# Optimization experiments

Measured on AMD Instinct MI355X. Metric: run time of the kernel, lower is better.

Reference implementation:

```python
import jax, jax.numpy as jnp
import numpy as np

B, S, E, H = 4, 1024, 1024, 16
HD = E // H

def setup_inputs() -> dict:
    key = jax.random.key(0)
    ks = jax.random.split(key, 12)
    std = 1.0 / np.sqrt(E)
    inp = {
        "query": jax.random.normal(ks[0], (B, S, E), jnp.float32),
        "key_t": jax.random.normal(ks[1], (B, S, E), jnp.float32),
        "value": jax.random.normal(ks[2], (B, S, E), jnp.float32),
        # causal mask, broadcastable to (B, H, S, S); 0 => masked
        "mask": jnp.tril(jnp.ones((S, S), jnp.int32))[None, None],
        "Wq": jax.random.normal(ks[3], (E, E), jnp.float32) * std,
        "bq": jnp.zeros((E,), jnp.float32),
        "Wk": jax.random.normal(ks[4], (E, E), jnp.float32) * std,
        "bk": jnp.zeros((E,), jnp.float32),
        "Wv": jax.random.normal(ks[5], (E, E), jnp.float32) * std,
        "bv": jnp.zeros((E,), jnp.float32),
        "Wo": jax.random.normal(ks[6], (E, E), jnp.float32) * std,
        "bo": jnp.zeros((E,), jnp.float32),
    }
    return inp

def reference(query, key_t, value, mask, Wq, bq, Wk, bk, Wv, bv, Wo, bo):
    scale = jnp.asarray(np.sqrt(HD), query.dtype)
    # projections (torch Linear: x @ W.T + b), split into heads -> (B, H, S, HD)
    def split_heads(x):
        return x.reshape(B, S, H, HD).transpose(0, 2, 1, 3)
    q = split_heads(query @ Wq.T + bq)
    k = split_heads(key_t @ Wk.T + bk)
    v = split_heads(value @ Wv.T + bv)
    scores = jnp.einsum("bhqd,bhkd->bhqk", q, k) / scale  # (B,H,S,S)
    scores = jnp.where(mask == 0, jnp.asarray(-jnp.inf, scores.dtype), scores)
    attn = jax.nn.softmax(scores, axis=-1)
    # dropout is identity in eval / p=0
    out = jnp.einsum("bhqk,bhkd->bhqd", attn, v)
    out = out.transpose(0, 2, 1, 3).reshape(B, S, E)
    out = out @ Wo.T + bo
    return out, attn
```

## Files before the change

### kernel.cpp

```cpp
#include <hip/hip_runtime.h>
#include <hip/hip_bf16.h>


typedef short bf16x8 __attribute__((ext_vector_type(8)));
typedef float f32x4 __attribute__((ext_vector_type(4)));

__device__ __forceinline__ unsigned short f2bf(float f) {
  union { float f; unsigned u; } v; v.f = f;
  unsigned r = v.u + 0x7FFF + ((v.u >> 16) & 1);
  return (unsigned short)(r >> 16);
}

__device__ __forceinline__ void gload16(const unsigned short* g, unsigned short* l) {
  __builtin_amdgcn_global_load_lds(
      (const __attribute__((address_space(1))) unsigned int*)g,
      (__attribute__((address_space(3))) unsigned int*)l, 16, 0, 0);
}

__global__ __launch_bounds__(256) void cast3_k(
    const float* __restrict__ a, const float* __restrict__ b,
    const float* __restrict__ c,
    unsigned short* __restrict__ oa, unsigned short* __restrict__ ob,
    unsigned short* __restrict__ oc) {
  const float* in = blockIdx.y == 0 ? a : blockIdx.y == 1 ? b : c;
  unsigned short* out = blockIdx.y == 0 ? oa : blockIdx.y == 1 ? ob : oc;
  int i = (blockIdx.x * 256 + threadIdx.x) * 8;
  float4 x = *(const float4*)(in + i);
  float4 y = *(const float4*)(in + i + 4);
  unsigned short t[8] = { f2bf(x.x), f2bf(x.y), f2bf(x.z), f2bf(x.w),
                          f2bf(y.x), f2bf(y.y), f2bf(y.z), f2bf(y.w) };
  *(bf16x8*)(out + i) = *(bf16x8*)t;
}

__global__ __launch_bounds__(256) void cast4_k(
    const float* __restrict__ a, const float* __restrict__ b,
    const float* __restrict__ c, const float* __restrict__ d,
    unsigned short* __restrict__ oa, unsigned short* __restrict__ ob,
    unsigned short* __restrict__ oc, unsigned short* __restrict__ od) {
  const float* in = blockIdx.y == 0 ? a : blockIdx.y == 1 ? b : blockIdx.y == 2 ? c : d;
  unsigned short* out = blockIdx.y == 0 ? oa : blockIdx.y == 1 ? ob : blockIdx.y == 2 ? oc : od;
  int i = (blockIdx.x * 256 + threadIdx.x) * 8;
  float4 x = *(const float4*)(in + i);
  float4 y = *(const float4*)(in + i + 4);
  unsigned short t[8] = { f2bf(x.x), f2bf(x.y), f2bf(x.z), f2bf(x.w),
                          f2bf(y.x), f2bf(y.y), f2bf(y.z), f2bf(y.w) };
  *(bf16x8*)(out + i) = *(bf16x8*)t;
}

__device__ __forceinline__ void gemm_core(
    const unsigned short* __restrict__ A, const unsigned short* __restrict__ W,
    int m0, int n0, int K, unsigned short* As, unsigned short* Bs, f32x4 acc[4][4])
{
  const int tid = threadIdx.x;
  const int w = tid >> 6, lane = tid & 63, quad = lane >> 4, lc = lane & 15;
  const int wm = (w >> 1) * 64, wn = (w & 1) * 64;
  const int lrow = lane >> 3, lg = lane & 7;

  for (int kb = 0; kb < K; kb += 64) {
#pragma unroll
    for (int t = 0; t < 4; t++) {
      int row = w * 32 + t * 8 + lrow;
      int gsw = lg ^ (row & 7);
      gload16(&A[(size_t)(m0 + row) * K + kb + gsw * 8], &As[(w * 32 + t * 8) * 64]);
      gload16(&W[(size_t)(n0 + row) * K + kb + gsw * 8], &Bs[(w * 32 + t * 8) * 64]);
    }
    __syncthreads();
#pragma unroll
    for (int kk = 0; kk < 2; kk++) {
      bf16x8 af[4], bfr[4];
#pragma unroll
      for (int i = 0; i < 4; i++) {
        int ra = wm + i * 16 + lc;
        af[i] = *(const bf16x8*)&As[ra * 64 + (((kk * 4 + quad) ^ (ra & 7)) * 8)];
      }
#pragma unroll
      for (int j = 0; j < 4; j++) {
        int rb = wn + j * 16 + lc;
        bfr[j] = *(const bf16x8*)&Bs[rb * 64 + (((kk * 4 + quad) ^ (rb & 7)) * 8)];
      }
#pragma unroll
      for (int i = 0; i < 4; i++)
#pragma unroll
        for (int j = 0; j < 4; j++)
          acc[i][j] = __builtin_amdgcn_mfma_f32_16x16x32_bf16(af[i], bfr[j], acc[i][j], 0, 0, 0);
    }
    __syncthreads();
  }
}

__global__ __launch_bounds__(256) void gemm_qkv(
    const unsigned short* __restrict__ Xq, const unsigned short* __restrict__ Xk,
    const unsigned short* __restrict__ Xv,
    const unsigned short* __restrict__ Wq, const unsigned short* __restrict__ Wk,
    const unsigned short* __restrict__ Wv,
    const float* __restrict__ bq, const float* __restrict__ bk, const float* __restrict__ bv,
    unsigned short* __restrict__ Qb, unsigned short* __restrict__ Kb,
    unsigned short* __restrict__ Vt)
{
  __shared__ __align__(16) unsigned short S[128 * 136];
  unsigned short* As = S;
  unsigned short* Bs = S + 128 * 64;
  const int z = blockIdx.z;
  const unsigned short* A = z == 0 ? Xq : z == 1 ? Xk : Xv;
  const unsigned short* W = z == 0 ? Wq : z == 1 ? Wk : Wv;
  const float* bias = z == 0 ? bq : z == 1 ? bk : bv;
  unsigned short* outRM = z == 0 ? Qb : Kb;
  const int m0 = blockIdx.x * 128, n0 = blockIdx.y * 128;
  const int tid = threadIdx.x;
  const int w = tid >> 6, lane = tid & 63, quad = lane >> 4, lc = lane & 15;
  const int wm = (w >> 1) * 64, wn = (w & 1) * 64;

  f32x4 acc[4][4] = {};
  gemm_core(A, W, m0, n0, 1024, As, Bs, acc);

  if (z < 2) {
#pragma unroll
    for (int j = 0; j < 4; j++) {
      int col = n0 + wn + j * 16 + lc;
      float bvl = bias[col];
#pragma unroll
      for (int i = 0; i < 4; i++)
#pragma unroll
        for (int r = 0; r < 4; r++) {
          int row = m0 + wm + i * 16 + quad * 4 + r;
          outRM[(size_t)row * 1024 + col] = f2bf(acc[i][j][r] + bvl);
        }
    }
  } else {
    unsigned short* T = S;
#pragma unroll
    for (int j = 0; j < 4; j++) {
      int col = wn + j * 16 + lc;
      float bvl = bias[n0 + col];
#pragma unroll
      for (int i = 0; i < 4; i++)
#pragma unroll
        for (int r = 0; r < 4; r++) {
          int row = wm + i * 16 + quad * 4 + r;
          T[col * 136 + (((row >> 3) ^ (col & 7)) << 3) + (row & 7)] =
              f2bf(acc[i][j][r] + bvl);
        }
    }
    __syncthreads();
    const int b_ = m0 >> 10, sb = m0 & 1023;
#pragma unroll
    for (int it = 0; it < 8; it++) {
      int cl = w * 32 + it * 4 + (lane >> 4);
      int sg = lane & 15;
      int colg = n0 + cl;
      *(bf16x8*)&Vt[((size_t)((b_ * 16 + (colg >> 6)) * 64 + (colg & 63))) * 1024 + sb + sg * 8] =
          *(const bf16x8*)&T[cl * 136 + ((sg ^ (cl & 7)) << 3)];
    }
  }
}

__global__ __launch_bounds__(256) void gemm_out(
    const unsigned short* __restrict__ A, const unsigned short* __restrict__ W,
    const float* __restrict__ bias, float* __restrict__ outf)
{
  __shared__ __align__(16) unsigned short As[128 * 64];
  __shared__ __align__(16) unsigned short Bs[128 * 64];
  const int m0 = blockIdx.x * 128, n0 = blockIdx.y * 128;
  const int tid = threadIdx.x;
  const int w = tid >> 6, lane = tid & 63, quad = lane >> 4, lc = lane & 15;
  const int wm = (w >> 1) * 64, wn = (w & 1) * 64;

  f32x4 acc[4][4] = {};
  gemm_core(A, W, m0, n0, 1024, As, Bs, acc);

#pragma unroll
  for (int j = 0; j < 4; j++) {
    int col = n0 + wn + j * 16 + lc;
    float bvl = bias[col];
#pragma unroll
    for (int i = 0; i < 4; i++)
#pragma unroll
      for (int r = 0; r < 4; r++) {
        int row = m0 + wm + i * 16 + quad * 4 + r;
        outf[(size_t)row * 1024 + col] = acc[i][j][r] + bvl;
      }
  }
}

__global__ __launch_bounds__(256) void attn_fused(
    const unsigned short* __restrict__ Qb,
    const unsigned short* __restrict__ Kb,
    const unsigned short* __restrict__ Vt,
    float* __restrict__ attn,
    unsigned short* __restrict__ O)
{
  __shared__ __align__(16) unsigned short Ks[64 * 64];
  __shared__ __align__(16) unsigned short Vs[64 * 64];
  __shared__ __align__(16) unsigned short Pl[4][16][40];
  __shared__ __align__(16) float          Ps[4][16][36];
  const int bh = blockIdx.x, b = bh >> 4, h = bh & 15;
  const int by = (int)gridDim.y - 1 - (int)blockIdx.y;
  const int q0 = by * 64;
  const int tid = threadIdx.x;
  const int w = tid >> 6, lane = tid & 63, quad = lane >> 4, lc = lane & 15;
  const int g0 = q0 + w * 16;
  const int kt_d = g0 >> 4;
  const int nch = by + 1;
  const int sr = lane >> 3, sg = lane & 7;

  const unsigned short* qp = Qb + ((size_t)(b * 1024 + g0 + lc)) * 1024 + h * 64 + quad * 8;
  bf16x8 a0 = *(const bf16x8*)qp;
  bf16x8 a1 = *(const bf16x8*)(qp + 32);

  float m_[4] = { -1e30f, -1e30f, -1e30f, -1e30f };
  float l_[4] = { 0.f, 0.f, 0.f, 0.f };

  for (int c = 0; c < nch; c++) {
    int kv0 = c * 64;
    {
      int r0 = w * 8 + sr, r1 = 32 + r0;
      gload16(&Kb[((size_t)(b * 1024 + kv0 + r0)) * 1024 + h * 64 + (sg ^ (r0 & 7)) * 8],
              &Ks[(w * 8) * 64]);
      gload16(&Kb[((size_t)(b * 1024 + kv0 + r1)) * 1024 + h * 64 + (sg ^ (r1 & 7)) * 8],
              &Ks[(32 + w * 8) * 64]);
    }
    __syncthreads();
    int tmax = kt_d - c * 4;
    int tlim = tmax < 3 ? tmax : 3;
    for (int t = 0; t <= tlim; t++) {
      int rk = t * 16 + lc;
      const unsigned short* kr = &Ks[rk * 64];
      bf16x8 b0 = *(const bf16x8*)&kr[((quad ^ (rk & 7))) * 8];
      bf16x8 b1 = *(const bf16x8*)&kr[(((quad + 4) ^ (rk & 7))) * 8];
      f32x4 cc = {};
      cc = __builtin_amdgcn_mfma_f32_16x16x32_bf16(a0, b0, cc, 0, 0, 0);
      cc = __builtin_amdgcn_mfma_f32_16x16x32_bf16(a1, b1, cc, 0, 0, 0);
      if (t < tmax) {
#pragma unroll
        for (int r = 0; r < 4; r++) {
          float s = cc[r] * 0.125f;
          float mn = fmaxf(m_[r], s);
          l_[r] = l_[r] * __expf(m_[r] - mn) + __expf(s - mn);
          m_[r] = mn;
        }
      } else {
#pragma unroll
        for (int r = 0; r < 4; r++) {
          int qr = g0 + quad * 4 + r;
          float sv = (kv0 + t * 16 + lc) > qr ? -1e30f : cc[r] * 0.125f;
          float mn = fmaxf(m_[r], sv);
          l_[r] = l_[r] * __expf(m_[r] - mn) + __expf(sv - mn);
          m_[r] = mn;
        }
      }
    }
    __syncthreads();
  }

  float mofs[4];
#pragma unroll
  for (int r = 0; r < 4; r++) {
    float mT = m_[r];
#pragma unroll
    for (int off = 1; off < 16; off <<= 1) mT = fmaxf(mT, __shfl_xor(mT, off));
    float lt = l_[r] * __expf(m_[r] - mT);
#pragma unroll
    for (int off = 1; off < 16; off <<= 1) lt += __shfl_xor(lt, off);
    mofs[r] = mT + __logf(lt);
  }

  float* arow = attn + (size_t)bh * 1024 * 1024;
  f32x4 oacc[4] = {};
  for (int c = 0; c < nch; c++) {
    int kv0 = c * 64;
    {
      int r0 = w * 8 + sr, r1 = 32 + r0;
      gload16(&Kb[((size_t)(b * 1024 + kv0 + r0)) * 1024 + h * 64 + (sg ^ (r0 & 7)) * 8],
              &Ks[(w * 8) * 64]);
      gload16(&Kb[((size_t)(b * 1024 + kv0 + r1)) * 1024 + h * 64 + (sg ^ (r1 & 7)) * 8],
              &Ks[(32 + w * 8) * 64]);
      gload16(&Vt[((size_t)(bh * 64 + r0)) * 1024 + kv0 + (sg ^ (r0 & 7)) * 8],
              &Vs[(w * 8) * 64]);
      gload16(&Vt[((size_t)(bh * 64 + r1)) * 1024 + kv0 + (sg ^ (r1 & 7)) * 8],
              &Vs[(32 + w * 8) * 64]);
    }
    __syncthreads();
    int tmax = kt_d - c * 4;
#pragma unroll
    for (int u = 0; u < 2; u++) {
      if (u * 2 <= tmax) {
#pragma unroll
        for (int t2 = 0; t2 < 2; t2++) {
          int t = u * 2 + t2;
          if (t <= tmax) {
            int rk = t * 16 + lc;
            const unsigned short* kr = &Ks[rk * 64];
            bf16x8 b0 = *(const bf16x8*)&kr[((quad ^ (rk & 7))) * 8];
            bf16x8 b1 = *(const bf16x8*)&kr[(((quad + 4) ^ (rk & 7))) * 8];
            f32x4 cc = {};
            cc = __builtin_amdgcn_mfma_f32_16x16x32_bf16(a0, b0, cc, 0, 0, 0);
            cc = __builtin_amdgcn_mfma_f32_16x16x32_bf16(a1, b1, cc, 0, 0, 0);
#pragma unroll
            for (int r = 0; r < 4; r++) {
              int qr = g0 + quad * 4 + r;
              float p = (kv0 + t * 16 + lc) > qr ? 0.f : __expf(cc[r] * 0.125f - mofs[r]);
              Ps[w][quad * 4 + r][t2 * 16 + lc] = p;
              Pl[w][quad * 4 + r][t2 * 16 + lc] = f2bf(p);
            }
          } else {
#pragma unroll
            for (int r = 0; r < 4; r++) Pl[w][quad * 4 + r][t2 * 16 + lc] = 0;
          }
        }
        bf16x8 pa = *(const bf16x8*)&Pl[w][lc][quad * 8];
#pragma unroll
        for (int j = 0; j < 4; j++) {
          int hd = j * 16 + lc;
          bf16x8 bv = *(const bf16x8*)&Vs[hd * 64 + (((u * 4 + quad) ^ (hd & 7)) * 8)];
          oacc[j] = __builtin_amdgcn_mfma_f32_16x16x32_bf16(pa, bv, oacc[j], 0, 0, 0);
        }
        int nt = tmax - u * 2 + 1; if (nt > 2) nt = 2;
        int srow = lane >> 2, cf = (lane & 3) * 4;
        float* dst = &arow[(size_t)(g0 + srow) * 1024 + kv0 + u * 32];
        *(float4*)(dst + cf) = *(const float4*)&Ps[w][srow][cf];
        if (nt == 2)
          *(float4*)(dst + 16 + cf) = *(const float4*)&Ps[w][srow][16 + cf];
      }
    }
    __syncthreads();
  }

  {
    int rr = lane >> 3, cl = lane & 7;
    float4 z = make_float4(0.f, 0.f, 0.f, 0.f);
#pragma unroll
    for (int half = 0; half < 2; half++) {
      float* rowp = &arow[(size_t)(g0 + half * 8 + rr) * 1024];
      for (int c0 = g0 + 16 + cl * 4; c0 < 1024; c0 += 32)
        *(float4*)(rowp + c0) = z;
    }
  }

  {
    unsigned short* ob = (unsigned short*)&Ps[w][0][0];
#pragma unroll
    for (int j = 0; j < 4; j++)
#pragma unroll
      for (int r = 0; r < 4; r++)
        ob[(quad * 4 + r) * 72 + j * 16 + lc] = f2bf(oacc[j][r]);
#pragma unroll
    for (int it = 0; it < 2; it++) {
      int row = it * 8 + (lane >> 3), off = (lane & 7) * 8;
      *(bf16x8*)&O[((size_t)(b * 1024 + g0 + row)) * 1024 + h * 64 + off] =
          *(const bf16x8*)&ob[row * 72 + off];
    }
  }
}

extern "C" void kernel_launch(void* const* d_in, const int* in_sizes, int n_in,
                              void* d_out, int out_size, void* d_ws, size_t ws_size,
                              hipStream_t stream) {
  const float* query = (const float*)d_in[0];
  const float* key_t = (const float*)d_in[1];
  const float* value = (const float*)d_in[2];
  const float* Wq = (const float*)d_in[4];
  const float* bq = (const float*)d_in[5];
  const float* Wk = (const float*)d_in[6];
  const float* bk = (const float*)d_in[7];
  const float* Wv = (const float*)d_in[8];
  const float* bv = (const float*)d_in[9];
  const float* Wo = (const float*)d_in[10];
  const float* bo = (const float*)d_in[11];

  unsigned short* Xq  = (unsigned short*)d_ws;
  unsigned short* Xk  = Xq  + 4194304;
  unsigned short* Xv  = Xk  + 4194304;
  unsigned short* Wqb = Xv  + 4194304;
  unsigned short* Wkb = Wqb + 1048576;
  unsigned short* Wvb = Wkb + 1048576;
  unsigned short* Wob = Wvb + 1048576;
  unsigned short* Qb  = Wob + 1048576;
  unsigned short* Kb  = Qb  + 4194304;
  unsigned short* Vtb = Kb  + 4194304;
  unsigned short* Ob  = Vtb + 4194304;

  float* outO = (float*)d_out;
  float* attn = outO + 4194304;

  cast3_k<<<dim3(2048, 3), 256, 0, stream>>>(query, key_t, value, Xq, Xk, Xv);
  cast4_k<<<dim3(512, 4), 256, 0, stream>>>(Wq, Wk, Wv, Wo, Wqb, Wkb, Wvb, Wob);

  gemm_qkv<<<dim3(32, 8, 3), 256, 0, stream>>>(Xq, Xk, Xv, Wqb, Wkb, Wvb,
                                               bq, bk, bv, Qb, Kb, Vtb);

  attn_fused<<<dim3(64, 16), 256, 0, stream>>>(Qb, Kb, Vtb, attn, Ob);

  gemm_out<<<dim3(32, 8), 256, 0, stream>>>(Ob, Wob, bo, outO);
}
```

Baseline: 469.5 us.

## Merge cast kernels, use exp2 softmax, and drop fp32 probability staging buffer

Result: no change. 472.1 us (+0.5%).

```diff
diff --git a/kernel.cpp b/kernel.cpp
--- a/kernel.cpp
+++ b/kernel.cpp
@@ -4,6 +4,8 @@
 
 typedef short bf16x8 __attribute__((ext_vector_type(8)));
 typedef float f32x4 __attribute__((ext_vector_type(4)));
+
+#define SCALE2 0.18033688011112042f
 
 __device__ __forceinline__ unsigned short f2bf(float f) {
   union { float f; unsigned u; } v; v.f = f;
@@ -11,35 +13,36 @@
   return (unsigned short)(r >> 16);
 }
 
+__device__ __forceinline__ float bf2f(unsigned short u) {
+  union { unsigned u; float f; } v; v.u = ((unsigned)u) << 16;
+  return v.f;
+}
+
 __device__ __forceinline__ void gload16(const unsigned short* g, unsigned short* l) {
   __builtin_amdgcn_global_load_lds(
       (const __attribute__((address_space(1))) unsigned int*)g,
       (__attribute__((address_space(3))) unsigned int*)l, 16, 0, 0);
 }
 
-__global__ __launch_bounds__(256) void cast3_k(
-    const float* __restrict__ a, const float* __restrict__ b,
-    const float* __restrict__ c,
-    unsigned short* __restrict__ oa, unsigned short* __restrict__ ob,
-    unsigned short* __restrict__ oc) {
-  const float* in = blockIdx.y == 0 ? a : blockIdx.y == 1 ? b : c;
-  unsigned short* out = blockIdx.y == 0 ? oa : blockIdx.y == 1 ? ob : oc;
-  int i = (blockIdx.x * 256 + threadIdx.x) * 8;
-  float4 x = *(const float4*)(in + i);
-  float4 y = *(const float4*)(in + i + 4);
-  unsigned short t[8] = { f2bf(x.x), f2bf(x.y), f2bf(x.z), f2bf(x.w),
-                          f2bf(y.x), f2bf(y.y), f2bf(y.z), f2bf(y.w) };
-  *(bf16x8*)(out + i) = *(bf16x8*)t;
-}
-
-__global__ __launch_bounds__(256) void cast4_k(
-    const float* __restrict__ a, const float* __restrict__ b,
-    const float* __restrict__ c, const float* __restrict__ d,
-    unsigned short* __restrict__ oa, unsigned short* __restrict__ ob,
-    unsigned short* __restrict__ oc, unsigned short* __restrict__ od) {
-  const float* in = blockIdx.y == 0 ? a : blockIdx.y == 1 ? b : blockIdx.y == 2 ? c : d;
-  unsigned short* out = blockIdx.y == 0 ? oa : blockIdx.y == 1 ? ob : blockIdx.y == 2 ? oc : od;
-  int i = (blockIdx.x * 256 + threadIdx.x) * 8;
+__global__ __launch_bounds__(256) void cast_all(
+    const float* __restrict__ q, const float* __restrict__ k, const float* __restrict__ v,
+    const float* __restrict__ w0, const float* __restrict__ w1,
+    const float* __restrict__ w2, const float* __restrict__ w3,
+    unsigned short* __restrict__ oq, unsigned short* __restrict__ ok,
+    unsigned short* __restrict__ ov, unsigned short* __restrict__ o0,
+    unsigned short* __restrict__ o1, unsigned short* __restrict__ o2,
+    unsigned short* __restrict__ o3) {
+  const float* in; unsigned short* out; int i;
+  if (blockIdx.y < 3) {
+    in  = blockIdx.y == 0 ? q : blockIdx.y == 1 ? k : v;
+    out = blockIdx.y == 0 ? oq : blockIdx.y == 1 ? ok : ov;
+    i = (blockIdx.x * 256 + threadIdx.x) * 8;
+  } else {
+    int ws = blockIdx.x >> 9;
+    in  = ws == 0 ? w0 : ws == 1 ? w1 : ws == 2 ? w2 : w3;
+    out = ws == 0 ? o0 : ws == 1 ? o1 : ws == 2 ? o2 : o3;
+    i = ((blockIdx.x & 511) * 256 + threadIdx.x) * 8;
+  }
   float4 x = *(const float4*)(in + i);
   float4 y = *(const float4*)(in + i + 4);
   unsigned short t[8] = { f2bf(x.x), f2bf(x.y), f2bf(x.z), f2bf(x.w),
@@ -189,15 +192,15 @@
     float* __restrict__ attn,
     unsigned short* __restrict__ O)
 {
-  __shared__ __align__(16) unsigned short Ks[64 * 64];
-  __shared__ __align__(16) unsigned short Vs[64 * 64];
-  __shared__ __align__(16) unsigned short Pl[4][16][40];
-  __shared__ __align__(16) float          Ps[4][16][36];
+  __shared__ __align__(16) unsigned short SM[10752];
+  unsigned short* Ks = SM;
+  unsigned short* Vs = SM + 4096;
   const int bh = blockIdx.x, b = bh >> 4, h = bh & 15;
   const int by = (int)gridDim.y - 1 - (int)blockIdx.y;
   const int q0 = by * 64;
   const int tid = threadIdx.x;
   const int w = tid >> 6, lane = tid & 63, quad = lane >> 4, lc = lane & 15;
+  unsigned short* Plw = SM + 8192 + w * 640;
   const int g0 = q0 + w * 16;
   const int kt_d = g0 >> 4;
   const int nch = by + 1;
@@ -233,18 +236,18 @@
       if (t < tmax) {
 #pragma unroll
         for (int r = 0; r < 4; r++) {
-          float s = cc[r] * 0.125f;
+          float s = cc[r] * SCALE2;
           float mn = fmaxf(m_[r], s);
-          l_[r] = l_[r] * __expf(m_[r] - mn) + __expf(s - mn);
+          l_[r] = l_[r] * exp2f(m_[r] - mn) + exp2f(s - mn);
           m_[r] = mn;
         }
       } else {
 #pragma unroll
         for (int r = 0; r < 4; r++) {
           int qr = g0 + quad * 4 + r;
-          float sv = (kv0 + t * 16 + lc) > qr ? -1e30f : cc[r] * 0.125f;
+          float sv = (kv0 + t * 16 + lc) > qr ? -1e30f : cc[r] * SCALE2;
           float mn = fmaxf(m_[r], sv);
-          l_[r] = l_[r] * __expf(m_[r] - mn) + __expf(sv - mn);
+          l_[r] = l_[r] * exp2f(m_[r] - mn) + exp2f(sv - mn);
           m_[r] = mn;
         }
       }
@@ -258,10 +261,10 @@
     float mT = m_[r];
 #pragma unroll
     for (int off = 1; off < 16; off <<= 1) mT = fmaxf(mT, __shfl_xor(mT, off));
-    float lt = l_[r] * __expf(m_[r] - mT);
+    float lt = l_[r] * exp2f(m_[r] - mT);
 #pragma unroll
     for (int off = 1; off < 16; off <<= 1) lt += __shfl_xor(lt, off);
-    mofs[r] = mT + __logf(lt);
+    mofs[r] = mT + __log2f(lt);
   }
 
   float* arow = attn + (size_t)bh * 1024 * 1024;
@@ -298,28 +301,34 @@
 #pragma unroll
             for (int r = 0; r < 4; r++) {
               int qr = g0 + quad * 4 + r;
-              float p = (kv0 + t * 16 + lc) > qr ? 0.f : __expf(cc[r] * 0.125f - mofs[r]);
-              Ps[w][quad * 4 + r][t2 * 16 + lc] = p;
-              Pl[w][quad * 4 + r][t2 * 16 + lc] = f2bf(p);
+              float p = (kv0 + t * 16 + lc) > qr ? 0.f
+                        : exp2f(cc[r] * SCALE2 - mofs[r]);
+              Plw[(quad * 4 + r) * 40 + t2 * 16 + lc] = f2bf(p);
             }
           } else {
 #pragma unroll
-            for (int r = 0; r < 4; r++) Pl[w][quad * 4 + r][t2 * 16 + lc] = 0;
+            for (int r = 0; r < 4; r++) Plw[(quad * 4 + r) * 40 + t2 * 16 + lc] = 0;
           }
         }
-        bf16x8 pa = *(const bf16x8*)&Pl[w][lc][quad * 8];
+        bf16x8 pa = *(const bf16x8*)&Plw[lc * 40 + quad * 8];
 #pragma unroll
         for (int j = 0; j < 4; j++) {
           int hd = j * 16 + lc;
           bf16x8 bv = *(const bf16x8*)&Vs[hd * 64 + (((u * 4 + quad) ^ (hd & 7)) * 8)];
           oacc[j] = __builtin_amdgcn_mfma_f32_16x16x32_bf16(pa, bv, oacc[j], 0, 0, 0);
         }
-        int nt = tmax - u * 2 + 1; if (nt > 2) nt = 2;
-        int srow = lane >> 2, cf = (lane & 3) * 4;
-        float* dst = &arow[(size_t)(g0 + srow) * 1024 + kv0 + u * 32];
-        *(float4*)(dst + cf) = *(const float4*)&Ps[w][srow][cf];
-        if (nt == 2)
-          *(float4*)(dst + 16 + cf) = *(const float4*)&Ps[w][srow][16 + cf];
+        {
+          int srow8 = lane >> 3, c8 = lane & 7;
+#pragma unroll
+          for (int hf = 0; hf < 2; hf++) {
+            int row = hf * 8 + srow8;
+            const unsigned short* ps = &Plw[row * 40 + c8 * 4];
+            f32x4 fv;
+            fv[0] = bf2f(ps[0]); fv[1] = bf2f(ps[1]);
+            fv[2] = bf2f(ps[2]); fv[3] = bf2f(ps[3]);
+            *(f32x4*)&arow[(size_t)(g0 + row) * 1024 + kv0 + u * 32 + c8 * 4] = fv;
+          }
+        }
       }
     }
     __syncthreads();
@@ -337,7 +346,7 @@
   }
 
   {
-    unsigned short* ob = (unsigned short*)&Ps[w][0][0];
+    unsigned short* ob = SM + w * 1152;
 #pragma unroll
     for (int j = 0; j < 4; j++)
 #pragma unroll
@@ -382,8 +391,8 @@
   float* outO = (float*)d_out;
   float* attn = outO + 4194304;
 
-  cast3_k<<<dim3(2048, 3), 256, 0, stream>>>(query, key_t, value, Xq, Xk, Xv);
-  cast4_k<<<dim3(512, 4), 256, 0, stream>>>(Wq, Wk, Wv, Wo, Wqb, Wkb, Wvb, Wob);
+  cast_all<<<dim3(2048, 4), 256, 0, stream>>>(query, key_t, value, Wq, Wk, Wv, Wo,
+                                              Xq, Xk, Xv, Wqb, Wkb, Wvb, Wob);
 
   gemm_qkv<<<dim3(32, 8, 3), 256, 0, stream>>>(Xq, Xk, Xv, Wqb, Wkb, Wvb,
                                                bq, bk, bv, Qb, Kb, Vtb);
```
